# Kernel tuning notes

Measured on AMD Instinct MI355X. Metric: run time of the kernel, lower is better.

The kernel has to match this reference:

```python
import jax, jax.numpy as jnp
import numpy as np

EMBED = 256
HEADS = 8
LEVELS = 3
POINTS = 4
MLP = 4
SS = np.array([[100, 100], [50, 50], [25, 25]], np.int32)  # (H, W) per level


def setup_inputs() -> dict:
    key = jax.random.key(0)
    ks = jax.random.split(key, 12)
    B, Q = 2, 128 * 128
    NV = int((SS[:, 0] * SS[:, 1]).sum())
    C = EMBED
    F = C * MLP
    s = 0.02

    def w(k, shape):
        return jax.random.normal(k, shape, jnp.float32) * s

    return dict(
        query=jax.random.normal(ks[0], (B, Q, C), jnp.float32),
        value=jax.random.normal(ks[1], (B, NV, C), jnp.float32),
        query_pos=jax.random.normal(ks[2], (B, Q, C), jnp.float32),
        ref_pts=jax.random.uniform(ks[3], (B, Q, 2), jnp.float32),
        spatial_shapes=SS,
        level_start_index=np.concatenate([[0], np.cumsum(SS[:, 0] * SS[:, 1])[:-1]]).astype(np.int32),
        ln1_g=jnp.ones(C), ln1_b=jnp.zeros(C),
        ln2_g=jnp.ones(C), ln2_b=jnp.zeros(C),
        W_value=w(ks[4], (C, C)), b_value=jnp.zeros(C),
        W_off=w(ks[5], (C, HEADS * LEVELS * POINTS * 2)), b_off=w(ks[6], (HEADS * LEVELS * POINTS * 2,)),
        W_attn=w(ks[7], (C, HEADS * LEVELS * POINTS)), b_attn=jnp.zeros(HEADS * LEVELS * POINTS),
        W_out=w(ks[8], (C, C)), b_out=jnp.zeros(C),
        W_ffn1=w(ks[9], (C, F)), b_ffn1=jnp.zeros(F),
        W_ffn2=w(ks[10], (F, C)), b_ffn2=jnp.zeros(C),
    )


def _layernorm(x, g, b, eps=1e-5):
    m = x.mean(-1, keepdims=True)
    v = ((x - m) ** 2).mean(-1, keepdims=True)
    return (x - m) * jax.lax.rsqrt(v + eps) * g + b


def _bilinear(v, loc, Hl, Wl):
    # v: [BH, Hl*Wl, d]; loc: [BH, Q, P, 2] normalized to [0,1].
    # grid_sample(align_corners=False, padding=zeros): pixel = loc*size - 0.5
    BH, Q, P, _ = loc.shape
    d = v.shape[-1]
    x = loc[..., 0] * Wl - 0.5
    y = loc[..., 1] * Hl - 0.5
    x0f = jnp.floor(x)
    y0f = jnp.floor(y)
    lx = x - x0f
    ly = y - y0f
    x0 = x0f.astype(jnp.int32)
    y0 = y0f.astype(jnp.int32)

    def gather(xi, yi):
        valid = ((xi >= 0) & (xi < Wl) & (yi >= 0) & (yi < Hl)).astype(v.dtype)
        idx = jnp.clip(yi, 0, Hl - 1) * Wl + jnp.clip(xi, 0, Wl - 1)
        g = jnp.take_along_axis(v, idx.reshape(BH, Q * P, 1), axis=1).reshape(BH, Q, P, d)
        return g * valid[..., None]

    w00 = (1 - lx) * (1 - ly)
    w01 = lx * (1 - ly)
    w10 = (1 - lx) * ly
    w11 = lx * ly
    return (gather(x0, y0) * w00[..., None] + gather(x0 + 1, y0) * w01[..., None]
            + gather(x0, y0 + 1) * w10[..., None] + gather(x0 + 1, y0 + 1) * w11[..., None])


def _forward(query, value, query_pos, ref_pts, spatial_shapes,
             ln1_g, ln1_b, ln2_g, ln2_b,
             W_value, b_value, W_off, b_off, W_attn, b_attn, W_out, b_out,
             W_ffn1, b_ffn1, W_ffn2, b_ffn2):
    B, Q, C = query.shape
    Hh, L, P = HEADS, LEVELS, POINTS
    d = C // Hh
    ss = np.asarray(spatial_shapes)
    starts = np.concatenate([[0], np.cumsum(ss[:, 0] * ss[:, 1])])

    # pre-norm + positional embedding (MSDeformAttn adds query_pos)
    qn = _layernorm(query, ln1_g, ln1_b)
    q = qn + query_pos

    # value projection, split heads
    v = (value @ W_value + b_value).reshape(B, -1, Hh, d)

    off = (q @ W_off + b_off).reshape(B, Q, Hh, L, P, 2)
    aw = jax.nn.softmax((q @ W_attn + b_attn).reshape(B, Q, Hh, L * P), axis=-1)
    aw = aw.reshape(B, Q, Hh, L, P)

    # offset normalizer is (W, H) per level
    normalizer = jnp.asarray(ss[:, ::-1].copy(), jnp.float32)
    # bev_value path: ref_pts broadcast over levels
    loc = ref_pts[:, :, None, None, None, :] + off / normalizer[None, None, None, :, None, :]

    out = jnp.zeros((B * Hh, Q, d), query.dtype)
    for l in range(L):
        Hl, Wl = int(ss[l, 0]), int(ss[l, 1])
        v_l = v[:, starts[l]:starts[l + 1]].transpose(0, 2, 1, 3).reshape(B * Hh, Hl * Wl, d)
        loc_l = loc[:, :, :, l].transpose(0, 2, 1, 3, 4).reshape(B * Hh, Q, P, 2)
        sampled = _bilinear(v_l, loc_l, Hl, Wl)  # [BH, Q, P, d]
        w_l = aw[:, :, :, l].transpose(0, 2, 1, 3).reshape(B * Hh, Q, P)
        out = out + (sampled * w_l[..., None]).sum(2)

    out = out.reshape(B, Hh, Q, d).transpose(0, 2, 1, 3).reshape(B, Q, C)
    x = query + (out @ W_out + b_out)

    h = _layernorm(x, ln2_g, ln2_b)
    x = x + (jax.nn.gelu(h @ W_ffn1 + b_ffn1, approximate=False) @ W_ffn2 + b_ffn2)
    return x


def reference(query, value, query_pos, ref_pts, spatial_shapes, level_start_index,
              ln1_g, ln1_b, ln2_g, ln2_b,
              W_value, b_value, W_off, b_off, W_attn, b_attn, W_out, b_out,
              W_ffn1, b_ffn1, W_ffn2, b_ffn2):
    return _forward(query, value, query_pos, ref_pts, spatial_shapes,
                    ln1_g, ln1_b, ln2_g, ln2_b,
                    W_value, b_value, W_off, b_off, W_attn, b_attn, W_out, b_out,
                    W_ffn1, b_ffn1, W_ffn2, b_ffn2)
```

## Files before the change

### kernel.cpp

```cpp
#include <hip/hip_runtime.h>
#include <hip/hip_bf16.h>

#define BQ      2
#define QLEN    16384
#define CDIM    256
#define HEADS   8
#define LEV     3
#define PTS     4
#define DHEAD   32
#define NVTOT   13125
#define FDIM    1024
#define NTOK    (BQ*QLEN)
#define MROWS_V (BQ*NVTOT)
#define NPROJ   288

typedef __attribute__((ext_vector_type(8))) short short8;
typedef __attribute__((ext_vector_type(4))) float floatx4;
typedef unsigned long long u64;

typedef const __attribute__((address_space(1))) unsigned int gu32;
typedef __attribute__((address_space(3))) unsigned int lu32;

__device__ __forceinline__ int imin(int a, int b){ return a<b?a:b; }
__device__ __forceinline__ int imax(int a, int b){ return a>b?a:b; }

__device__ __forceinline__ float bf2f(unsigned short u){ return __uint_as_float((unsigned)u << 16); }
__device__ __forceinline__ unsigned short f2bf(float f)
{
    __hip_bfloat16 h = __float2bfloat16(f);
    return *(unsigned short*)&h;
}
__device__ __forceinline__ u64 pack4(float4 v)
{
    return (u64)f2bf(v.x) | ((u64)f2bf(v.y) << 16)
         | ((u64)f2bf(v.z) << 32) | ((u64)f2bf(v.w) << 48);
}
__device__ __forceinline__ float4 unpack4(u64 c)
{
    float4 v;
    v.x = bf2f((unsigned short)(c));
    v.y = bf2f((unsigned short)(c >> 16));
    v.z = bf2f((unsigned short)(c >> 32));
    v.w = bf2f((unsigned short)(c >> 48));
    return v;
}

__device__ __forceinline__ float gelu_f(float x)
{
    float u2 = x * x;
    float a  = x * fmaf(0.0713548163f, u2, 1.5957691216f);
    float e  = __expf(a);
    float r  = __builtin_amdgcn_rcpf(e + 1.0f);
    return fmaf(-x, r, x);
}

__device__ __forceinline__ void ln_core(float4 v, const float* __restrict__ pos, int tok,
                                        const float* __restrict__ g, const float* __restrict__ b,
                                        int lane, __hip_bfloat16* __restrict__ out)
{
    float s = v.x + v.y + v.z + v.w;
    #pragma unroll
    for (int o = 32; o > 0; o >>= 1) s += __shfl_down(s, o);
    s = __shfl(s, 0);
    float mean = s * (1.0f / 256.0f);
    float4 c; c.x = v.x - mean; c.y = v.y - mean; c.z = v.z - mean; c.w = v.w - mean;
    float q2 = c.x*c.x + c.y*c.y + c.z*c.z + c.w*c.w;
    #pragma unroll
    for (int o = 32; o > 0; o >>= 1) q2 += __shfl_down(q2, o);
    q2 = __shfl(q2, 0);
    float rstd = rsqrtf(q2 * (1.0f / 256.0f) + 1e-5f);
    float4 gg = ((const float4*)g)[lane];
    float4 bb = ((const float4*)b)[lane];
    float4 o4;
    o4.x = c.x * rstd * gg.x + bb.x;
    o4.y = c.y * rstd * gg.y + bb.y;
    o4.z = c.z * rstd * gg.z + bb.z;
    o4.w = c.w * rstd * gg.w + bb.w;
    if (pos) {
        float4 p = ((const float4*)(pos + (size_t)tok * CDIM))[lane];
        o4.x += p.x; o4.y += p.y; o4.z += p.z; o4.w += p.w;
    }
    *(u64*)(out + (size_t)tok * CDIM + lane * 4) = pack4(o4);
}

#define WT_BLOCKS  2946
#define CVT_BLOCKS 6563
#define LN_BLOCKS  8192

__global__ __launch_bounds__(256)
void prep_k(const float* __restrict__ Wv,  const float* __restrict__ Woff,
            const float* __restrict__ Wat, const float* __restrict__ Wout,
            const float* __restrict__ W1,  const float* __restrict__ W2,
            const float* __restrict__ boff, const float* __restrict__ bat,
            const float* __restrict__ value, const float* __restrict__ query,
            const float* __restrict__ qpos,  const float* __restrict__ ln1g,
            const float* __restrict__ ln1b,
            __hip_bfloat16* __restrict__ o_v,  __hip_bfloat16* __restrict__ o_c,
            __hip_bfloat16* __restrict__ o_out,
            __hip_bfloat16* __restrict__ o_1,  __hip_bfloat16* __restrict__ o_2,
            float* __restrict__ o_bc,
            __hip_bfloat16* __restrict__ vbf,  __hip_bfloat16* __restrict__ qbf)
{
    int bx = blockIdx.x;
    if (bx < WT_BLOCKS) {
        int gid = bx * 256 + threadIdx.x;
        if (gid < 65536) {
            int idx = gid, n = idx >> 8, k = idx & 255;
            o_v[idx] = __float2bfloat16(Wv[(size_t)k * 256 + n]);
        } else if (gid < 163840) {
            int idx = gid - 65536, n = idx >> 8, k = idx & 255;
            float v = 0.0f;
            if (n < 192)       v = Woff[(size_t)k * 192 + n];
            else if (n < 288)  v = Wat[(size_t)k * 96 + (n - 192)];
            o_c[idx] = __float2bfloat16(v);
        } else if (gid < 229376) {
            int idx = gid - 163840, n = idx >> 8, k = idx & 255;
            o_out[idx] = __float2bfloat16(Wout[(size_t)k * 256 + n]);
        } else if (gid < 491520) {
            int idx  = gid - 229376;
            int e    = idx & 7;
            int c    = idx >> 3;
            int lane = c & 63, lm = lane & 15, lk = lane >> 4;
            int r    = (c >> 6) & 15;
            int wn   = (c >> 10) & 3;
            int fc   = c >> 12;
            int i    = r & 1, ks = (r >> 1) & 1, kt = r >> 2;
            int row  = fc * 128 + wn * 32 + i * 16 + lm;
            int col  = kt * 64 + ks * 32 + lk * 8 + e;
            o_1[idx] = __float2bfloat16(W1[(size_t)col * 1024 + row]);
        } else if (gid < 753664) {
            int idx  = gid - 491520;
            int e    = idx & 7;
            int c    = idx >> 3;
            int lane = c & 63, lm = lane & 15, lk = lane >> 4;
            int r    = (c >> 6) & 15;
            int wn   = (c >> 10) & 3;
            int fc   = c >> 12;
            int i2   = r & 3, ks2 = r >> 2;
            int row  = wn * 64 + i2 * 16 + lm;
            int col  = fc * 128 + ks2 * 32 + lk * 8 + e;
            o_2[idx] = __float2bfloat16(W2[(size_t)col * 256 + row]);
        } else if (gid < 753952) {
            int idx = gid - 753664;
            o_bc[idx] = (idx < 192) ? boff[idx] : bat[idx - 192];
        }
    } else if (bx < WT_BLOCKS + CVT_BLOCKS) {
        int i = (bx - WT_BLOCKS) * 256 + threadIdx.x;
        if (i < MROWS_V * CDIM / 4) {
            float4 v = ((const float4*)value)[i];
            *(u64*)(vbf + (size_t)i * 4) = pack4(v);
        }
    } else {
        int tok  = (bx - WT_BLOCKS - CVT_BLOCKS) * 4 + (threadIdx.x >> 6);
        int lane = threadIdx.x & 63;
        float4 v = ((const float4*)(query + (size_t)tok * CDIM))[lane];
        ln_core(v, qpos, tok, ln1g, ln1b, lane, qbf);
    }
}

__global__ __launch_bounds__(256)
void ln2_k(const __hip_bfloat16* __restrict__ x, const float* __restrict__ g,
           const float* __restrict__ b, __hip_bfloat16* __restrict__ out)
{
    int tok  = blockIdx.x * 4 + (threadIdx.x >> 6);
    int lane = threadIdx.x & 63;
    float4 v = unpack4(((const u64*)(x + (size_t)tok * CDIM))[lane]);
    ln_core(v, nullptr, tok, g, b, lane, out);
}

enum { EP_PLAIN_BF16 = 0, EP_GELU_BF16 = 1, EP_RES_F2BF = 2, EP_RES_BF2F = 3 };

__global__ __launch_bounds__(256)
void mm_k(const __hip_bfloat16* __restrict__ A, const __hip_bfloat16* __restrict__ Bt,
          const float* __restrict__ bias, const void* __restrict__ res,
          void* __restrict__ Cout, int M, int N, int K, int mode)
{
    __shared__ float4 smem4[2048];
    __hip_bfloat16* Ws = (__hip_bfloat16*)smem4;
    __hip_bfloat16* Ts = (__hip_bfloat16*)smem4 + 128*64;
    u64* st = (u64*)smem4;
    int t = threadIdx.x;
    int lane = t & 63;
    int wave = t >> 6;
    int wm = wave >> 1, wn = wave & 1;
    int lm = lane & 15, lk = lane >> 4;
    int m0 = blockIdx.x * 128;
    int n0 = blockIdx.y * 128;

    floatx4 acc[4][4];
    #pragma unroll
    for (int i = 0; i < 4; i++)
        #pragma unroll
        for (int j = 0; j < 4; j++) acc[i][j] = (floatx4)0.0f;

    for (int kt = 0; kt < K; kt += 64) {
        #pragma unroll
        for (int i = 0; i < 4; i++) {
            int cc  = i * 256 + t;
            int row = cc >> 3;
            int c   = cc & 7;
            int kc  = c ^ (row & 7);
            int ra  = m0 + row; if (ra >= M) ra = M - 1;
            const __hip_bfloat16* gw = Bt + (size_t)(n0 + row) * K + kt + kc * 8;
            const __hip_bfloat16* gt = A  + (size_t)ra * K + kt + kc * 8;
            __builtin_amdgcn_global_load_lds((gu32*)gw, (lu32*)(Ws + cc * 8), 16, 0, 0);
            __builtin_amdgcn_global_load_lds((gu32*)gt, (lu32*)(Ts + cc * 8), 16, 0, 0);
        }
        __syncthreads();
        #pragma unroll
        for (int ks = 0; ks < 2; ks++) {
            short8 wf[4], tf[4];
            #pragma unroll
            for (int i = 0; i < 4; i++) {
                int rw = wn * 64 + i * 16 + lm;
                int cw = (ks * 4 + lk) ^ (rw & 7);
                wf[i] = *(const short8*)(Ws + (rw * 8 + cw) * 8);
                int rt = wm * 64 + i * 16 + lm;
                int ct = (ks * 4 + lk) ^ (rt & 7);
                tf[i] = *(const short8*)(Ts + (rt * 8 + ct) * 8);
            }
            #pragma unroll
            for (int i = 0; i < 4; i++)
                #pragma unroll
                for (int j = 0; j < 4; j++)
                    acc[i][j] = __builtin_amdgcn_mfma_f32_16x16x32_bf16(wf[i], tf[j], acc[i][j], 0, 0, 0);
        }
        __syncthreads();
    }

    #pragma unroll
    for (int i = 0; i < 4; i++) {
        int chan = n0 + wn * 64 + i * 16 + lk * 4;
        float4 b4 = make_float4(0.f, 0.f, 0.f, 0.f);
        if (chan < N) b4 = *(const float4*)(bias + chan);
        int c4 = wn * 16 + i * 4 + lk;
        #pragma unroll
        for (int j = 0; j < 4; j++) {
            int tl = wm * 64 + j * 16 + lm;
            float4 v;
            v.x = acc[i][j][0] + b4.x;
            v.y = acc[i][j][1] + b4.y;
            v.z = acc[i][j][2] + b4.z;
            v.w = acc[i][j][3] + b4.w;
            st[tl * 32 + (c4 ^ (tl & 31))] = pack4(v);
        }
    }
    __syncthreads();

    int rel = (t & 31) * 4;
    int c4r = t & 31;
    #pragma unroll
    for (int it = 0; it < 16; it++) {
        int tl   = it * 8 + (t >> 5);
        int tok  = m0 + tl;
        int chan = n0 + rel;
        if (tok >= M || chan >= N) continue;
        u64 chunk = st[tl * 32 + (c4r ^ (tl & 31))];
        if (mode == EP_PLAIN_BF16) {
            *(u64*)((__hip_bfloat16*)Cout + (size_t)tok * N + chan) = chunk;
        } else if (mode == EP_GELU_BF16) {
            float4 v = unpack4(chunk);
            v.x = gelu_f(v.x); v.y = gelu_f(v.y); v.z = gelu_f(v.z); v.w = gelu_f(v.w);
            *(u64*)((__hip_bfloat16*)Cout + (size_t)tok * N + chan) = pack4(v);
        } else if (mode == EP_RES_F2BF) {
            float4 v = unpack4(chunk);
            float4 rr = *(const float4*)((const float*)res + (size_t)tok * N + chan);
            v.x += rr.x; v.y += rr.y; v.z += rr.z; v.w += rr.w;
            *(u64*)((__hip_bfloat16*)Cout + (size_t)tok * N + chan) = pack4(v);
        } else {
            float4 v = unpack4(chunk);
            float4 rr = unpack4(*(const u64*)((const __hip_bfloat16*)res + (size_t)tok * N + chan));
            v.x += rr.x; v.y += rr.y; v.z += rr.z; v.w += rr.w;
            *(float4*)((float*)Cout + (size_t)tok * N + chan) = v;
        }
    }
}

__global__ __launch_bounds__(512, 1)
void ffn_k(const __hip_bfloat16* __restrict__ h,
           const __hip_bfloat16* __restrict__ W1p,
           const float* __restrict__ b1,
           const __hip_bfloat16* __restrict__ W2p,
           const float* __restrict__ b2,
           const __hip_bfloat16* __restrict__ xres,
           float* __restrict__ out)
{
    extern __shared__ char smem_dyn[];
    __hip_bfloat16* As = (__hip_bfloat16*)smem_dyn;

    int t    = threadIdx.x;
    int lane = t & 63;
    int wave = t >> 6;
    int wm   = wave >> 2;
    int wn   = wave & 3;
    int lm   = lane & 15, lk = lane >> 4;
    int m0   = blockIdx.x * 128;

    const short8* W1v = (const short8*)W1p;
    const short8* W2v = (const short8*)W2p;
    int wb = wn * 1024 + lane;

    #pragma unroll
    for (int i = 0; i < 8; i++) {
        int cc  = i * 512 + t;
        int kt  = cc >> 10;
        int rem = cc & 1023;
        int row = rem >> 3;
        int c   = rem & 7;
        int kc  = c ^ (row & 7);
        const __hip_bfloat16* src = h + (size_t)(m0 + row) * 256 + kt * 64 + kc * 8;
        __builtin_amdgcn_global_load_lds((gu32*)src, (lu32*)(As + cc * 8), 16, 0, 0);
    }

    floatx4 acc2[4][4];
    #pragma unroll
    for (int i = 0; i < 4; i++)
        #pragma unroll
        for (int j = 0; j < 4; j++) acc2[i][j] = (floatx4)0.0f;

    short8 w1c[16];
    #pragma unroll
    for (int r = 0; r < 16; r++) w1c[r] = W1v[wb + r * 64];

    __syncthreads();

    #pragma unroll 1
    for (int fc = 0; fc < 8; fc++) {
        int f0 = fc * 128;
        __hip_bfloat16* gs = (__hip_bfloat16*)(smem_dyn + 65536 + (fc & 1) * 32768);

        floatx4 acc1[2][4];
        #pragma unroll
        for (int i = 0; i < 2; i++)
            #pragma unroll
            for (int j = 0; j < 4; j++) acc1[i][j] = (floatx4)0.0f;

        #pragma unroll
        for (int kt = 0; kt < 4; kt++) {
            #pragma unroll
            for (int ks = 0; ks < 2; ks++) {
                short8 tf[4];
                #pragma unroll
                for (int j = 0; j < 4; j++) {
                    int rt = wm * 64 + j * 16 + lm;
                    int ct = (ks * 4 + lk) ^ (rt & 7);
                    tf[j] = *(const short8*)(As + (kt * 1024 + rt * 8 + ct) * 8);
                }
                #pragma unroll
                for (int i = 0; i < 2; i++)
                    #pragma unroll
                    for (int j = 0; j < 4; j++)
                        acc1[i][j] = __builtin_amdgcn_mfma_f32_16x16x32_bf16(
                            w1c[kt * 4 + ks * 2 + i], tf[j], acc1[i][j], 0, 0, 0);
            }
        }

        #pragma unroll
        for (int i = 0; i < 2; i++) {
            float4 bb = *(const float4*)(b1 + f0 + wn * 32 + i * 16 + lk * 4);
            int c = wn * 4 + i * 2 + (lk >> 1);
            #pragma unroll
            for (int j = 0; j < 4; j++) {
                int tok = wm * 64 + j * 16 + lm;
                float4 v;
                v.x = gelu_f(acc1[i][j][0] + bb.x);
                v.y = gelu_f(acc1[i][j][1] + bb.y);
                v.z = gelu_f(acc1[i][j][2] + bb.z);
                v.w = gelu_f(acc1[i][j][3] + bb.w);
                int sc = c ^ (tok & 7);
                *(u64*)((char*)gs + tok * 256 + sc * 16 + (lk & 1) * 8) = pack4(v);
            }
        }

        short8 w2f[16];
        #pragma unroll
        for (int r = 0; r < 16; r++) w2f[r] = W2v[fc * 4096 + wb + r * 64];

        int fcn = (fc < 7) ? fc + 1 : 7;
        #pragma unroll
        for (int r = 0; r < 16; r++) w1c[r] = W1v[fcn * 4096 + wb + r * 64];

        __syncthreads();

        #pragma unroll
        for (int ks2 = 0; ks2 < 4; ks2++) {
            short8 tf2[4];
            #pragma unroll
            for (int j = 0; j < 4; j++) {
                int tok = wm * 64 + j * 16 + lm;
                int sc = (ks2 * 4 + lk) ^ (tok & 7);
                tf2[j] = *(const short8*)((char*)gs + tok * 256 + sc * 16);
            }
            #pragma unroll
            for (int i2 = 0; i2 < 4; i2++)
                #pragma unroll
                for (int j = 0; j < 4; j++)
                    acc2[i2][j] = __builtin_amdgcn_mfma_f32_16x16x32_bf16(
                        w2f[ks2 * 4 + i2], tf2[j], acc2[i2][j], 0, 0, 0);
        }
    }

    #pragma unroll
    for (int i2 = 0; i2 < 4; i2++) {
        int c0 = wn * 64 + i2 * 16 + lk * 4;
        float4 bb = *(const float4*)(b2 + c0);
        #pragma unroll
        for (int j = 0; j < 4; j++) {
            int tok = m0 + wm * 64 + j * 16 + lm;
            float4 r = unpack4(*(const u64*)(xres + (size_t)tok * 256 + c0));
            float4 v;
            v.x = acc2[i2][j][0] + bb.x + r.x;
            v.y = acc2[i2][j][1] + bb.y + r.y;
            v.z = acc2[i2][j][2] + bb.z + r.z;
            v.w = acc2[i2][j][3] + bb.w + r.w;
            *(float4*)(out + (size_t)tok * 256 + c0) = v;
        }
    }
}

__global__ __launch_bounds__(256, 6)
void sample_k(const __hip_bfloat16* __restrict__ v, const __hip_bfloat16* __restrict__ cbuf,
              const float* __restrict__ ref, __hip_bfloat16* __restrict__ out)
{
    __shared__ int4   metaIdx[4 * 104];
    __shared__ float4 metaW[4 * 104];

    int wid  = threadIdx.x >> 6;
    int lane = threadIdx.x & 63;
    int t    = blockIdx.x * 4 + wid;
    int b    = t >> 14;
    float rx = ref[(size_t)t * 2 + 0];
    float ry = ref[(size_t)t * 2 + 1];
    const __hip_bfloat16* crow = cbuf + (size_t)t * NPROJ;

    #pragma unroll
    for (int rnd = 0; rnd < 2; rnd++) {
        int slot = rnd * 64 + lane;
        int h = slot >> 4, p = slot & 15;
        int pc = imin(p, 11);
        unsigned upk = *(const unsigned*)(crow + h * 24 + pc * 2);
        float ox = bf2f((unsigned short)upk);
        float oy = bf2f((unsigned short)(upk >> 16));
        float logit = bf2f(*(const unsigned short*)(crow + 192 + h * 12 + pc));
        float mx = logit;
        #pragma unroll
        for (int o = 8; o > 0; o >>= 1) mx = fmaxf(mx, __shfl_xor(mx, o, 16));
        float e = (p < 12) ? __expf(logit - mx) : 0.0f;
        float ssum = e;
        #pragma unroll
        for (int o = 8; o > 0; o >>= 1) ssum += __shfl_xor(ssum, o, 16);
        float aw = e * __builtin_amdgcn_rcpf(ssum);

        if (p < 12) {
            int l = p >> 2;
            float fS = (l == 0) ? 100.0f : ((l == 1) ? 50.0f : 25.0f);
            int   Wl = (l == 0) ? 100 : ((l == 1) ? 50 : 25);
            int   st = (l == 0) ? 0 : ((l == 1) ? 10000 : 12500);
            float x = fmaf(rx, fS, ox) - 0.5f;
            float y = fmaf(ry, fS, oy) - 0.5f;
            float x0f = floorf(x), y0f = floorf(y);
            float fx = x - x0f, fy = y - y0f;
            int x0 = (int)x0f, y0 = (int)y0f;
            int x1 = x0 + 1,  y1 = y0 + 1;
            int cx0 = imin(imax(x0, 0), Wl - 1), cx1 = imin(imax(x1, 0), Wl - 1);
            int cy0 = imin(imax(y0, 0), Wl - 1), cy1 = imin(imax(y1, 0), Wl - 1);
            float vx0 = (x0 >= 0 && x0 < Wl) ? 1.0f : 0.0f;
            float vx1 = (x1 >= 0 && x1 < Wl) ? 1.0f : 0.0f;
            float vy0 = (y0 >= 0 && y0 < Wl) ? 1.0f : 0.0f;
            float vy1 = (y1 >= 0 && y1 < Wl) ? 1.0f : 0.0f;
            int s = wid * 104 + h * 13 + p;
            metaIdx[s] = make_int4((st + cy0 * Wl + cx0) << 9, (st + cy0 * Wl + cx1) << 9,
                                   (st + cy1 * Wl + cx0) << 9, (st + cy1 * Wl + cx1) << 9);
            metaW[s] = make_float4((1.0f - fx) * (1.0f - fy) * aw * vx0 * vy0,
                                   fx * (1.0f - fy) * aw * vx1 * vy0,
                                   (1.0f - fx) * fy * aw * vx0 * vy1,
                                   fx * fy * aw * vx1 * vy1);
        }
    }
    __syncthreads();

    int h  = lane >> 3;
    int bs = __builtin_amdgcn_readfirstlane(b);
    const char* vb = (const char*)(v + (size_t)bs * NVTOT * CDIM);
    int hoff = lane * 8;
    int sB   = wid * 104 + h * 13;
    float4 acc = {0.0f, 0.0f, 0.0f, 0.0f};

    int4   miA = metaIdx[sB + 0];
    float4 mwA = metaW[sB + 0];
    u64 a0 = *(const u64*)(vb + (unsigned)(miA.x + hoff));
    u64 a1 = *(const u64*)(vb + (unsigned)(miA.y + hoff));
    u64 a2 = *(const u64*)(vb + (unsigned)(miA.z + hoff));
    u64 a3 = *(const u64*)(vb + (unsigned)(miA.w + hoff));
    int4   miB = metaIdx[sB + 1];
    float4 mwB = metaW[sB + 1];
    u64 b0 = *(const u64*)(vb + (unsigned)(miB.x + hoff));
    u64 b1 = *(const u64*)(vb + (unsigned)(miB.y + hoff));
    u64 b2 = *(const u64*)(vb + (unsigned)(miB.z + hoff));
    u64 b3 = *(const u64*)(vb + (unsigned)(miB.w + hoff));

    #pragma unroll
    for (int p = 0; p < 12; p++) {
        int pn = (p < 10) ? (p + 2) : 11;
        int4   miN = metaIdx[sB + pn];
        float4 mwN = metaW[sB + pn];
        u64 n0 = *(const u64*)(vb + (unsigned)(miN.x + hoff));
        u64 n1 = *(const u64*)(vb + (unsigned)(miN.y + hoff));
        u64 n2 = *(const u64*)(vb + (unsigned)(miN.z + hoff));
        u64 n3 = *(const u64*)(vb + (unsigned)(miN.w + hoff));

        {
            unsigned d0 = (unsigned)a0, d1 = (unsigned)(a0 >> 32);
            acc.x = fmaf(mwA.x, __uint_as_float(d0 << 16), acc.x);
            acc.y = fmaf(mwA.x, __uint_as_float(d0 & 0xffff0000u), acc.y);
            acc.z = fmaf(mwA.x, __uint_as_float(d1 << 16), acc.z);
            acc.w = fmaf(mwA.x, __uint_as_float(d1 & 0xffff0000u), acc.w);
        }
        {
            unsigned d0 = (unsigned)a1, d1 = (unsigned)(a1 >> 32);
            acc.x = fmaf(mwA.y, __uint_as_float(d0 << 16), acc.x);
            acc.y = fmaf(mwA.y, __uint_as_float(d0 & 0xffff0000u), acc.y);
            acc.z = fmaf(mwA.y, __uint_as_float(d1 << 16), acc.z);
            acc.w = fmaf(mwA.y, __uint_as_float(d1 & 0xffff0000u), acc.w);
        }
        {
            unsigned d0 = (unsigned)a2, d1 = (unsigned)(a2 >> 32);
            acc.x = fmaf(mwA.z, __uint_as_float(d0 << 16), acc.x);
            acc.y = fmaf(mwA.z, __uint_as_float(d0 & 0xffff0000u), acc.y);
            acc.z = fmaf(mwA.z, __uint_as_float(d1 << 16), acc.z);
            acc.w = fmaf(mwA.z, __uint_as_float(d1 & 0xffff0000u), acc.w);
        }
        {
            unsigned d0 = (unsigned)a3, d1 = (unsigned)(a3 >> 32);
            acc.x = fmaf(mwA.w, __uint_as_float(d0 << 16), acc.x);
            acc.y = fmaf(mwA.w, __uint_as_float(d0 & 0xffff0000u), acc.y);
            acc.z = fmaf(mwA.w, __uint_as_float(d1 << 16), acc.z);
            acc.w = fmaf(mwA.w, __uint_as_float(d1 & 0xffff0000u), acc.w);
        }

        a0 = b0; a1 = b1; a2 = b2; a3 = b3; mwA = mwB;
        b0 = n0; b1 = n1; b2 = n2; b3 = n3; mwB = mwN;
    }
    *(u64*)(out + (size_t)t * CDIM + lane * 4) = pack4(acc);
}

extern "C" void kernel_launch(void* const* d_in, const int* in_sizes, int n_in,
                              void* d_out, int out_size, void* d_ws, size_t ws_size,
                              hipStream_t stream)
{
    const float* query = (const float*)d_in[0];
    const float* value = (const float*)d_in[1];
    const float* qpos  = (const float*)d_in[2];
    const float* ref   = (const float*)d_in[3];
    const float* ln1g  = (const float*)d_in[6];
    const float* ln1b  = (const float*)d_in[7];
    const float* ln2g  = (const float*)d_in[8];
    const float* ln2b  = (const float*)d_in[9];
    const float* Wv    = (const float*)d_in[10];
    const float* bv    = (const float*)d_in[11];
    const float* Woff  = (const float*)d_in[12];
    const float* boff  = (const float*)d_in[13];
    const float* Wat   = (const float*)d_in[14];
    const float* bat   = (const float*)d_in[15];
    const float* Wout  = (const float*)d_in[16];
    const float* bout  = (const float*)d_in[17];
    const float* W1    = (const float*)d_in[18];
    const float* b1    = (const float*)d_in[19];
    const float* W2    = (const float*)d_in[20];
    const float* b2    = (const float*)d_in[21];
    float* out = (float*)d_out;
    char*  ws  = (char*)d_ws;

    static bool attr_set = false;
    if (!attr_set) {
        hipFuncSetAttribute((const void*)ffn_k,
                            hipFuncAttributeMaxDynamicSharedMemorySize, 131072);
        attr_set = true;
    }

    const size_t MB = 1024 * 1024;
    __hip_bfloat16* Wvt   = (__hip_bfloat16*)(ws + 0);
    __hip_bfloat16* Wct   = (__hip_bfloat16*)(ws + 131072);
    __hip_bfloat16* Woutt = (__hip_bfloat16*)(ws + 327680);
    __hip_bfloat16* W1t   = (__hip_bfloat16*)(ws + 458752);
    __hip_bfloat16* W2t   = (__hip_bfloat16*)(ws + 983040);
    float*          bcomb = (float*)(ws + 1507328);
    __hip_bfloat16* qbf   = (__hip_bfloat16*)(ws + 2  * MB);
    __hip_bfloat16* aoutb = (__hip_bfloat16*)(ws + 19 * MB);
    __hip_bfloat16* vbf   = (__hip_bfloat16*)(ws + 36 * MB);
    __hip_bfloat16* vbuf  = (__hip_bfloat16*)(ws + 50 * MB);
    __hip_bfloat16* xbf   = (__hip_bfloat16*)(ws + 64 * MB);
    __hip_bfloat16* cbuf  = (__hip_bfloat16*)(ws + 81 * MB);
    __hip_bfloat16* hbf   = qbf;

    prep_k<<<WT_BLOCKS + CVT_BLOCKS + LN_BLOCKS, 256, 0, stream>>>(
        Wv, Woff, Wat, Wout, W1, W2, boff, bat, value, query, qpos, ln1g, ln1b,
        Wvt, Wct, Woutt, W1t, W2t, bcomb, vbf, qbf);
    mm_k<<<dim3((MROWS_V + 127) / 128, 2), 256, 0, stream>>>(
        vbf, Wvt, bv, nullptr, vbuf, MROWS_V, 256, 256, EP_PLAIN_BF16);
    mm_k<<<dim3(NTOK / 128, 3), 256, 0, stream>>>(
        qbf, Wct, bcomb, nullptr, cbuf, NTOK, NPROJ, 256, EP_PLAIN_BF16);
    sample_k<<<NTOK / 4, 256, 0, stream>>>(vbuf, cbuf, ref, aoutb);
    mm_k<<<dim3(NTOK / 128, 2), 256, 0, stream>>>(
        aoutb, Woutt, bout, query, xbf, NTOK, 256, 256, EP_RES_F2BF);
    ln2_k<<<NTOK / 4, 256, 0, stream>>>(xbf, ln2g, ln2b, hbf);
    ffn_k<<<NTOK / 128, 512, 131072, stream>>>(hbf, W1t, b1, W2t, b2, xbf, out);
}
```

Measured before the change: 329.1 us.

## Fuse LayerNorm2 into FFN kernel and merge value/query projection GEMM launches

LayerNorm2 now runs inside the FFN kernel on the bf16 tile already staged in shared memory, which removes the separate ln2 launch and its full read/write pass over the activations. The value projection and the offset/attention projection GEMMs are merged into one launch using blockIdx.z, so the two independent GEMMs can share the GPU and pay one launch overhead. In exchange, the value-projection half launches blocks that exit immediately, and the FFN kernel gains an extra LayerNorm phase and barrier before its main loop.

```diff
diff --git a/kernel.cpp b/kernel.cpp
--- a/kernel.cpp
+++ b/kernel.cpp
@@ -13,6 +13,7 @@
 #define NTOK    (BQ*QLEN)
 #define MROWS_V (BQ*NVTOT)
 #define NPROJ   288
+#define VP_GX   206
 
 typedef __attribute__((ext_vector_type(8))) short short8;
 typedef __attribute__((ext_vector_type(4))) float floatx4;
@@ -158,24 +159,14 @@
     }
 }
 
-__global__ __launch_bounds__(256)
-void ln2_k(const __hip_bfloat16* __restrict__ x, const float* __restrict__ g,
-           const float* __restrict__ b, __hip_bfloat16* __restrict__ out)
-{
-    int tok  = blockIdx.x * 4 + (threadIdx.x >> 6);
-    int lane = threadIdx.x & 63;
-    float4 v = unpack4(((const u64*)(x + (size_t)tok * CDIM))[lane]);
-    ln_core(v, nullptr, tok, g, b, lane, out);
-}
-
 enum { EP_PLAIN_BF16 = 0, EP_GELU_BF16 = 1, EP_RES_F2BF = 2, EP_RES_BF2F = 3 };
 
-__global__ __launch_bounds__(256)
-void mm_k(const __hip_bfloat16* __restrict__ A, const __hip_bfloat16* __restrict__ Bt,
-          const float* __restrict__ bias, const void* __restrict__ res,
-          void* __restrict__ Cout, int M, int N, int K, int mode)
-{
-    __shared__ float4 smem4[2048];
+__device__ __forceinline__
+void mm_body(float4* smem4,
+             const __hip_bfloat16* __restrict__ A, const __hip_bfloat16* __restrict__ Bt,
+             const float* __restrict__ bias, const void* __restrict__ res,
+             void* __restrict__ Cout, int M, int N, int K, int mode)
+{
     __hip_bfloat16* Ws = (__hip_bfloat16*)smem4;
     __hip_bfloat16* Ts = (__hip_bfloat16*)smem4 + 128*64;
     u64* st = (u64*)smem4;
@@ -276,13 +267,37 @@
     }
 }
 
+__global__ __launch_bounds__(256)
+void mm_k(const __hip_bfloat16* __restrict__ A, const __hip_bfloat16* __restrict__ Bt,
+          const float* __restrict__ bias, const void* __restrict__ res,
+          void* __restrict__ Cout, int M, int N, int K, int mode)
+{
+    __shared__ float4 smem4[2048];
+    mm_body(smem4, A, Bt, bias, res, Cout, M, N, K, mode);
+}
+
+__global__ __launch_bounds__(256)
+void mmj_k(const __hip_bfloat16* __restrict__ vbf, const __hip_bfloat16* __restrict__ Wvt,
+           const float* __restrict__ bv, __hip_bfloat16* __restrict__ vbuf,
+           const __hip_bfloat16* __restrict__ qbf, const __hip_bfloat16* __restrict__ Wct,
+           const float* __restrict__ bcomb, __hip_bfloat16* __restrict__ cbuf)
+{
+    __shared__ float4 smem4[2048];
+    if (blockIdx.z == 0) {
+        if (blockIdx.x >= VP_GX || blockIdx.y >= 2) return;
+        mm_body(smem4, vbf, Wvt, bv, nullptr, vbuf, MROWS_V, 256, 256, EP_PLAIN_BF16);
+    } else {
+        mm_body(smem4, qbf, Wct, bcomb, nullptr, cbuf, NTOK, NPROJ, 256, EP_PLAIN_BF16);
+    }
+}
+
 __global__ __launch_bounds__(512, 1)
-void ffn_k(const __hip_bfloat16* __restrict__ h,
+void ffn_k(const __hip_bfloat16* __restrict__ x,
+           const float* __restrict__ ln2g, const float* __restrict__ ln2b,
            const __hip_bfloat16* __restrict__ W1p,
            const float* __restrict__ b1,
            const __hip_bfloat16* __restrict__ W2p,
            const float* __restrict__ b2,
-           const __hip_bfloat16* __restrict__ xres,
            float* __restrict__ out)
 {
     extern __shared__ char smem_dyn[];
@@ -308,7 +323,7 @@
         int row = rem >> 3;
         int c   = rem & 7;
         int kc  = c ^ (row & 7);
-        const __hip_bfloat16* src = h + (size_t)(m0 + row) * 256 + kt * 64 + kc * 8;
+        const __hip_bfloat16* src = x + (size_t)(m0 + row) * 256 + kt * 64 + kc * 8;
         __builtin_amdgcn_global_load_lds((gu32*)src, (lu32*)(As + cc * 8), 16, 0, 0);
     }
 
@@ -322,6 +337,38 @@
     #pragma unroll
     for (int r = 0; r < 16; r++) w1c[r] = W1v[wb + r * 64];
 
+    __syncthreads();
+
+    {
+        int kt_l = lane >> 4;
+        int c_l  = (lane & 15) >> 1;
+        int h_l  = lane & 1;
+        float4 g4 = ((const float4*)ln2g)[lane];
+        float4 b4 = ((const float4*)ln2b)[lane];
+        #pragma unroll 1
+        for (int tt = 0; tt < 16; tt++) {
+            int tk = wave * 16 + tt;
+            __hip_bfloat16* p = As + ((kt_l * 1024 + tk * 8 + (c_l ^ (tk & 7))) * 8 + h_l * 4);
+            float4 v = unpack4(*(const u64*)p);
+            float s = v.x + v.y + v.z + v.w;
+            float q = v.x*v.x + v.y*v.y + v.z*v.z + v.w*v.w;
+            #pragma unroll
+            for (int o = 32; o > 0; o >>= 1) {
+                s += __shfl_down(s, o);
+                q += __shfl_down(q, o);
+            }
+            s = __shfl(s, 0);
+            q = __shfl(q, 0);
+            float mean = s * (1.0f / 256.0f);
+            float var  = fmaf(-mean, mean, q * (1.0f / 256.0f));
+            float rstd = rsqrtf(var + 1e-5f);
+            v.x = (v.x - mean) * rstd * g4.x + b4.x;
+            v.y = (v.y - mean) * rstd * g4.y + b4.y;
+            v.z = (v.z - mean) * rstd * g4.z + b4.z;
+            v.w = (v.w - mean) * rstd * g4.w + b4.w;
+            *(u64*)p = pack4(v);
+        }
+    }
     __syncthreads();
 
     #pragma unroll 1
@@ -407,7 +454,7 @@
         #pragma unroll
         for (int j = 0; j < 4; j++) {
             int tok = m0 + wm * 64 + j * 16 + lm;
-            float4 r = unpack4(*(const u64*)(xres + (size_t)tok * 256 + c0));
+            float4 r = unpack4(*(const u64*)(x + (size_t)tok * 256 + c0));
             float4 v;
             v.x = acc2[i2][j][0] + bb.x + r.x;
             v.y = acc2[i2][j][1] + bb.y + r.y;
@@ -591,18 +638,14 @@
     __hip_bfloat16* vbuf  = (__hip_bfloat16*)(ws + 50 * MB);
     __hip_bfloat16* xbf   = (__hip_bfloat16*)(ws + 64 * MB);
     __hip_bfloat16* cbuf  = (__hip_bfloat16*)(ws + 81 * MB);
-    __hip_bfloat16* hbf   = qbf;
 
     prep_k<<<WT_BLOCKS + CVT_BLOCKS + LN_BLOCKS, 256, 0, stream>>>(
         Wv, Woff, Wat, Wout, W1, W2, boff, bat, value, query, qpos, ln1g, ln1b,
         Wvt, Wct, Woutt, W1t, W2t, bcomb, vbf, qbf);
-    mm_k<<<dim3((MROWS_V + 127) / 128, 2), 256, 0, stream>>>(
-        vbf, Wvt, bv, nullptr, vbuf, MROWS_V, 256, 256, EP_PLAIN_BF16);
-    mm_k<<<dim3(NTOK / 128, 3), 256, 0, stream>>>(
-        qbf, Wct, bcomb, nullptr, cbuf, NTOK, NPROJ, 256, EP_PLAIN_BF16);
+    mmj_k<<<dim3(256, 3, 2), 256, 0, stream>>>(
+        vbf, Wvt, bv, vbuf, qbf, Wct, bcomb, cbuf);
     sample_k<<<NTOK / 4, 256, 0, stream>>>(vbuf, cbuf, ref, aoutb);
     mm_k<<<dim3(NTOK / 128, 2), 256, 0, stream>>>(
         aoutb, Woutt, bout, query, xbf, NTOK, 256, 256, EP_RES_F2BF);
-    ln2_k<<<NTOK / 4, 256, 0, stream>>>(xbf, ln2g, ln2b, hbf);
-    ffn_k<<<NTOK / 128, 512, 131072, stream>>>(hbf, W1t, b1, W2t, b2, xbf, out);
-}
+    ffn_k<<<NTOK / 128, 512, 131072, stream>>>(xbf, ln2g, ln2b, W1t, b1, W2t, b2, out);
+}
```

After: 334.2 us. Within noise of the previous version (+1.5%).
